# Kernel tuning notes

Hardware: AMD Instinct MI355X
Metric: run time of the kernel (lower is better)

Reference implementation:

```python
import jax, jax.numpy as jnp
import numpy as np

NUM_NODES, NODE_F = 50000, 128
NUM_EDGES, EDGE_F = 500000, 128
B, N = 4096, 100
D = 64      # node_dim
T = 8       # time_dim
LN_EPS = 1e-5


def setup_inputs() -> dict:
    key = jax.random.key(0)
    ks = jax.random.split(key, 16)
    inp = {
        'src_neighbor_node_ids': jax.random.randint(ks[0], (B, N), 0, NUM_NODES),
        'src_neighbor_edge_ids': jax.random.randint(ks[1], (B, N), 0, NUM_EDGES),
        'src_neighbor_times': jax.random.uniform(ks[2], (B, N), dtype=jnp.float32),
        'dst_node_ids': jax.random.randint(ks[3], (B,), 0, NUM_NODES),
        'node_raw_features': jax.random.normal(ks[4], (NUM_NODES, NODE_F), jnp.float32),
        'edge_raw_features': jax.random.normal(ks[5], (NUM_EDGES, EDGE_F), jnp.float32),
        # projection layers (stored as [in, out])
        'W_feat': jax.random.normal(ks[6], (NODE_F, D), jnp.float32) / np.sqrt(NODE_F),
        'b_feat': jnp.zeros((D,), jnp.float32),
        'W_edge': jax.random.normal(ks[7], (1, D), jnp.float32),
        'b_edge': jnp.zeros((D,), jnp.float32),
        'W_time': jax.random.normal(ks[8], (T, D), jnp.float32) / np.sqrt(T),
        'b_time': jnp.zeros((D,), jnp.float32),
        'W_struct': jax.random.normal(ks[9], (1, D), jnp.float32),
        'b_struct': jnp.zeros((D,), jnp.float32),
        # time encoder (cosine basis with log-spaced frequencies)
        'w_tenc': (1.0 / 10 ** np.linspace(0, 9, T)).astype(np.float32),
        'b_tenc': jnp.zeros((T,), jnp.float32),
        # layernorm
        'ln_g': jnp.ones((D,), jnp.float32),
        'ln_b': jnp.zeros((D,), jnp.float32),
        # GCNConv
        'W_gcn': jax.random.normal(ks[10], (D, D), jnp.float32) / np.sqrt(D),
        'b_gcn': jnp.zeros((D,), jnp.float32),
        # output layer
        'W_out': jax.random.normal(ks[11], (D, D), jnp.float32) / np.sqrt(D),
        'b_out': jnp.zeros((D,), jnp.float32),
    }
    return inp


def reference(src_neighbor_node_ids, src_neighbor_edge_ids, src_neighbor_times,
              dst_node_ids, node_raw_features, edge_raw_features,
              W_feat, b_feat, W_edge, b_edge, W_time, b_time, W_struct, b_struct,
              w_tenc, b_tenc, ln_g, ln_b, W_gcn, b_gcn, W_out, b_out):
    f32 = jnp.float32
    nbr_raw = node_raw_features[src_neighbor_node_ids]            # [B,N,F]
    node_f = nbr_raw @ W_feat + b_feat                            # [B,N,D]
    edge_col = edge_raw_features[src_neighbor_edge_ids, 0][..., None]  # [B,N,1]
    edge_f = edge_col @ W_edge + b_edge
    t_enc = jnp.cos(src_neighbor_times[..., None] * w_tenc + b_tenc)   # [B,N,T]
    time_f = t_enc @ W_time + b_time
    co = (src_neighbor_node_ids == dst_node_ids[:, None]).astype(f32)[..., None]
    co_f = co @ W_struct + b_struct
    skill_nbr = nbr_raw[..., 0].astype(jnp.int32)                 # [B,N]
    skill_dst = node_raw_features[dst_node_ids, 0].astype(jnp.int32)  # [B]
    sim = (skill_nbr == skill_dst[:, None]).astype(f32)[..., None]
    sim_f = sim @ W_struct + b_struct
    fused = node_f + edge_f + time_f + co_f + sim_f               # [B,N,D]
    mu = fused.mean(-1, keepdims=True)
    var = ((fused - mu) ** 2).mean(-1, keepdims=True)
    fused = (fused - mu) * jax.lax.rsqrt(var + LN_EPS) * ln_g + ln_b
    # per-sample chain GCN: directed edges j -> j+1 for j in [0, v-2], v = #valid ids,
    # PyG gcn_norm with self loops: deg[j] = 1 + in_degree[j]
    h = fused @ W_gcn                                             # [B,N,D]
    v = (src_neighbor_node_ids > 0).sum(-1)                       # [B]
    pos = jnp.arange(N)[None, :]                                  # [1,N]
    has_in = ((pos >= 1) & (pos < v[:, None])).astype(f32)        # [B,N]
    deg = 1.0 + has_in
    dinv_sqrt = jax.lax.rsqrt(deg)
    h_prev = jnp.pad(h[:, :-1], ((0, 0), (1, 0), (0, 0)))
    d_prev = jnp.pad(dinv_sqrt[:, :-1], ((0, 0), (1, 0)))
    out = h / deg[..., None] + (has_in * d_prev * dinv_sqrt)[..., None] * h_prev + b_gcn
    gnn = jax.nn.relu(out)
    src_emb = gnn.mean(axis=1)                                    # [B,D] global_mean_pool over N
    dst_emb = node_raw_features[dst_node_ids] @ W_feat + b_feat
    src_emb = src_emb @ W_out + b_out
    dst_emb = dst_emb @ W_out + b_out
    return src_emb, dst_emb
```

## Files before the change

### kernel.cpp

```cpp
#include <hip/hip_runtime.h>
#include <stdint.h>

#define NUM_NODES 50000
#define B_ 4096
#define N_ 100

typedef float f32x4 __attribute__((ext_vector_type(4)));
typedef float f32x2 __attribute__((ext_vector_type(2)));
typedef int   i32x4 __attribute__((ext_vector_type(4)));
typedef short s16x8 __attribute__((ext_vector_type(8)));

__device__ inline unsigned short f2bf(float f) {
    unsigned u = __float_as_uint(f);
    u += 0x7fffu + ((u >> 16) & 1u);
    return (unsigned short)(u >> 16);
}

template <int CTRL>
__device__ inline float dpp_add(float x) {
    int t = __builtin_amdgcn_update_dpp(0, __float_as_int(x), CTRL, 0xf, 0xf, true);
    return x + __int_as_float(t);
}
__device__ inline float wave_sum64(float x) {
    x = dpp_add<0x111>(x);
    x = dpp_add<0x112>(x);
    x = dpp_add<0x114>(x);
    x = dpp_add<0x118>(x);
    x = dpp_add<0x142>(x);
    x = dpp_add<0x143>(x);
    return __int_as_float(__builtin_amdgcn_readlane(__float_as_int(x), 63));
}

__global__ __launch_bounds__(256) void k_pre(
    const float* __restrict__ node_raw, const float* __restrict__ W_feat,
    const float* __restrict__ b_feat, const float* __restrict__ W_gcn,
    const float* __restrict__ ln_g, const float* __restrict__ ln_b,
    const float* __restrict__ W_edge, const float* __restrict__ b_edge,
    const float* __restrict__ W_time, const float* __restrict__ b_time,
    const float* __restrict__ W_struct, const float* __restrict__ b_struct,
    float* __restrict__ proj, int* __restrict__ skill,
    float* __restrict__ hb, float* __restrict__ wmg, float* __restrict__ Mg,
    unsigned short* __restrict__ PGmF)
{
    __shared__ float red[4][64];
    __shared__ float PGms[12][64];
    __shared__ unsigned short WfB[16][64][8];
    int blk = blockIdx.x;
    int t = threadIdx.x;
    int dj = t & 63;

    if (blk == gridDim.x - 1) {
        int g = t >> 6;
        float acc = 0.f;
        #pragma unroll
        for (int i = 0; i < 16; ++i) {
            int dk = g * 16 + i;
            acc += ln_b[dk] * W_gcn[dk * 64 + dj];
        }
        red[g][dj] = acc;

        if (t < 64) {
            int d = t;
            float col[11];
            col[0] = W_edge[d];
            col[1] = W_struct[d];
            #pragma unroll
            for (int i = 0; i < 8; ++i) col[2 + i] = W_time[i * 64 + d];
            col[10] = b_edge[d] + b_time[d] + 2.f * b_struct[d];
            float wmv[11];
            #pragma unroll
            for (int j = 0; j < 11; ++j) wmv[j] = wave_sum64(col[j]) * (1.f / 64.f);
            float cc[11];
            #pragma unroll
            for (int j = 0; j < 11; ++j) cc[j] = col[j] - wmv[j];
            #pragma unroll
            for (int j = 0; j < 11; ++j) {
                #pragma unroll
                for (int k = j; k < 11; ++k) {
                    float m = wave_sum64(cc[j] * cc[k]);
                    if (t == 0) { Mg[j * 11 + k] = m; Mg[k * 11 + j] = m; }
                }
            }
            if (t == 0) {
                #pragma unroll
                for (int j = 0; j < 11; ++j) wmg[j] = wmv[j];
            }

            int j = t;
            float accp[12];
            #pragma unroll
            for (int m = 0; m < 12; ++m) accp[m] = 0.f;
            for (int d2 = 0; d2 < 64; ++d2) {
                float gg = ln_g[d2] * W_gcn[d2 * 64 + j];
                float bias_d = b_edge[d2] + b_time[d2] + 2.f * b_struct[d2];
                accp[0] = fmaf(W_edge[d2], gg, accp[0]);
                accp[1] = fmaf(W_struct[d2], gg, accp[1]);
                #pragma unroll
                for (int i = 0; i < 8; ++i)
                    accp[2 + i] = fmaf(W_time[i * 64 + d2], gg, accp[2 + i]);
                accp[10] = fmaf(bias_d, gg, accp[10]);
                accp[11] += gg;
            }
            #pragma unroll
            for (int m = 0; m < 12; ++m) PGms[m][j] = accp[m];
        }
        __syncthreads();
        if (g == 0) hb[dj] = red[0][dj] + red[1][dj] + red[2][dj] + red[3][dj];

        {
            int ct = t >> 6, l = t & 63;
            int col = ct * 16 + (l & 15);
            int ks = (l >> 4) * 8;
            s16x8 a2;
            #pragma unroll
            for (int j2 = 0; j2 < 8; ++j2) {
                int k = ks + j2;
                a2[j2] = (k < 12) ? (short)f2bf(PGms[k][col]) : (short)0;
            }
            *(s16x8*)(PGmF + ((size_t)ct * 64 + l) * 8) = a2;
        }
        return;
    }

    #pragma unroll
    for (int i = 0; i < 4; ++i) {
        int e = t + i * 256;
        int tile = e >> 6;
        int l = e & 63;
        int ct = tile >> 2, kt = tile & 3;
        int col = ct * 16 + (l & 15);
        int ks = kt * 32 + (l >> 4) * 8;
        s16x8 a;
        #pragma unroll
        for (int j = 0; j < 8; ++j)
            a[j] = (short)f2bf(W_feat[(ks + j) * 64 + col]);
        *(s16x8*)&WfB[tile][l][0] = a;
    }
    __syncthreads();

    int w = t >> 6, lane = t & 63;
    int rbase = blk * 64 + w * 16;
    int rA = rbase + (lane & 15);
    int rc = rA < NUM_NODES ? rA : (NUM_NODES - 1);
    int kq = lane >> 4;

    s16x8 A[4];
    float a0x = 0.f;
    #pragma unroll
    for (int kt = 0; kt < 4; ++kt) {
        const float* src = node_raw + (size_t)rc * 128 + kt * 32 + kq * 8;
        f32x4 v0 = *(const f32x4*)src;
        f32x4 v1 = *(const f32x4*)(src + 4);
        s16x8 a;
        a[0] = (short)f2bf(v0.x); a[1] = (short)f2bf(v0.y);
        a[2] = (short)f2bf(v0.z); a[3] = (short)f2bf(v0.w);
        a[4] = (short)f2bf(v1.x); a[5] = (short)f2bf(v1.y);
        a[6] = (short)f2bf(v1.z); a[7] = (short)f2bf(v1.w);
        A[kt] = a;
        if (kt == 0) a0x = v0.x;
    }
    if (kq == 0 && rA < NUM_NODES) skill[rA] = (int)a0x;

    f32x4 acc[4];
    #pragma unroll
    for (int ct = 0; ct < 4; ++ct) { f32x4 z = {0.f,0.f,0.f,0.f}; acc[ct] = z; }
    #pragma unroll
    for (int ct = 0; ct < 4; ++ct) {
        #pragma unroll
        for (int kt = 0; kt < 4; ++kt) {
            s16x8 bfr = *(const s16x8*)&WfB[ct * 4 + kt][lane][0];
            acc[ct] = __builtin_amdgcn_mfma_f32_16x16x32_bf16(A[kt], bfr, acc[ct], 0, 0, 0);
        }
    }
    #pragma unroll
    for (int ct = 0; ct < 4; ++ct) {
        int col = ct * 16 + (lane & 15);
        float bf = b_feat[col];
        #pragma unroll
        for (int j = 0; j < 4; ++j) {
            int row = rbase + kq * 4 + j;
            if (row < NUM_NODES)
                proj[(size_t)row * 64 + col] = acc[ct][j] + bf;
        }
    }
}

__global__ __launch_bounds__(256) void k_pg(
    const float* __restrict__ proj, const float* __restrict__ W_gcn,
    const float* __restrict__ ln_g,
    const float* __restrict__ W_out, const float* __restrict__ b_out,
    const float* __restrict__ W_edge, const float* __restrict__ b_edge,
    const float* __restrict__ W_time, const float* __restrict__ b_time,
    const float* __restrict__ W_struct, const float* __restrict__ b_struct,
    float* __restrict__ projG, float* __restrict__ dstE,
    float* __restrict__ stats)
{
    __shared__ unsigned short WgB[8][64][8];
    __shared__ unsigned short WoB[8][64][8];
    __shared__ unsigned short WsB[2][64][8];
    int t = threadIdx.x;

    #pragma unroll
    for (int i = 0; i < 2; ++i) {
        int e = t + i * 256;
        int tile = e >> 6, l = e & 63;
        int ct = tile >> 1, kt = tile & 1;
        int col = ct * 16 + (l & 15);
        int ks = kt * 32 + (l >> 4) * 8;
        s16x8 a, b2;
        #pragma unroll
        for (int j = 0; j < 8; ++j) {
            int k = ks + j;
            a[j]  = (short)f2bf(ln_g[k] * W_gcn[k * 64 + col]);
            b2[j] = (short)f2bf(W_out[k * 64 + col]);
        }
        *(s16x8*)&WgB[tile][l][0] = a;
        *(s16x8*)&WoB[tile][l][0] = b2;
    }
    if (t < 128) {
        int kt = t >> 6, l = t & 63;
        int col = l & 15;
        int ks = kt * 32 + (l >> 4) * 8;
        s16x8 a;
        #pragma unroll
        for (int j = 0; j < 8; ++j) {
            int d = ks + j;
            float v;
            if (col == 0) v = W_edge[d];
            else if (col == 1) v = W_struct[d];
            else if (col < 10) v = W_time[(col - 2) * 64 + d];
            else if (col == 10) v = b_edge[d] + b_time[d] + 2.f * b_struct[d];
            else if (col == 11) v = 1.f;
            else v = 0.f;
            a[j] = (short)f2bf(v);
        }
        *(s16x8*)&WsB[kt][l][0] = a;
    }
    __syncthreads();

    int w = t >> 6, lane = t & 63;
    int rbase = blockIdx.x * 64 + w * 16;
    int rA = rbase + (lane & 15);
    int rc = rA < NUM_NODES ? rA : (NUM_NODES - 1);
    int kq = lane >> 4;

    s16x8 Ahi[2], Alo[2], Qhi[2], Qlo[2];
    #pragma unroll
    for (int kt = 0; kt < 2; ++kt) {
        const float* src = proj + (size_t)rc * 64 + kt * 32 + kq * 8;
        f32x4 v0 = *(const f32x4*)src;
        f32x4 v1 = *(const f32x4*)(src + 4);
        #pragma unroll
        for (int j = 0; j < 8; ++j) {
            float v = (j < 4) ? v0[j] : v1[j - 4];
            unsigned short hi = f2bf(v);
            float rem = v - __uint_as_float((unsigned)hi << 16);
            Ahi[kt][j] = (short)hi;
            Alo[kt][j] = (short)f2bf(rem);
            float p2 = v * v;
            unsigned short h2 = f2bf(p2);
            float r2 = p2 - __uint_as_float((unsigned)h2 << 16);
            Qhi[kt][j] = (short)h2;
            Qlo[kt][j] = (short)f2bf(r2);
        }
    }

    f32x4 accG[4], accE[4];
    f32x4 accS = {0.f, 0.f, 0.f, 0.f}, accQ = {0.f, 0.f, 0.f, 0.f};
    #pragma unroll
    for (int ct = 0; ct < 4; ++ct) {
        f32x4 z = {0.f, 0.f, 0.f, 0.f};
        accG[ct] = z; accE[ct] = z;
    }
    #pragma unroll
    for (int ct = 0; ct < 4; ++ct) {
        #pragma unroll
        for (int kt = 0; kt < 2; ++kt) {
            s16x8 bg = *(const s16x8*)&WgB[ct * 2 + kt][lane][0];
            accG[ct] = __builtin_amdgcn_mfma_f32_16x16x32_bf16(Alo[kt], bg, accG[ct], 0, 0, 0);
            accG[ct] = __builtin_amdgcn_mfma_f32_16x16x32_bf16(Ahi[kt], bg, accG[ct], 0, 0, 0);
            s16x8 bo = *(const s16x8*)&WoB[ct * 2 + kt][lane][0];
            accE[ct] = __builtin_amdgcn_mfma_f32_16x16x32_bf16(Alo[kt], bo, accE[ct], 0, 0, 0);
            accE[ct] = __builtin_amdgcn_mfma_f32_16x16x32_bf16(Ahi[kt], bo, accE[ct], 0, 0, 0);
        }
    }
    #pragma unroll
    for (int kt = 0; kt < 2; ++kt) {
        s16x8 bs = *(const s16x8*)&WsB[kt][lane][0];
        accS = __builtin_amdgcn_mfma_f32_16x16x32_bf16(Alo[kt], bs, accS, 0, 0, 0);
        accS = __builtin_amdgcn_mfma_f32_16x16x32_bf16(Ahi[kt], bs, accS, 0, 0, 0);
        accQ = __builtin_amdgcn_mfma_f32_16x16x32_bf16(Qlo[kt], bs, accQ, 0, 0, 0);
        accQ = __builtin_amdgcn_mfma_f32_16x16x32_bf16(Qhi[kt], bs, accQ, 0, 0, 0);
    }

    #pragma unroll
    for (int ct = 0; ct < 4; ++ct) {
        int col = ct * 16 + (lane & 15);
        float bo_ = b_out[col];
        #pragma unroll
        for (int j = 0; j < 4; ++j) {
            int row = rbase + kq * 4 + j;
            if (row < NUM_NODES) {
                projG[(size_t)row * 64 + col] = accG[ct][j];
                dstE[(size_t)row * 64 + col] = accE[ct][j] + bo_;
            }
        }
    }
    int c = lane & 15;
    if (c <= 11) {
        #pragma unroll
        for (int j = 0; j < 4; ++j) {
            int row = rbase + kq * 4 + j;
            if (row < NUM_NODES) stats[(size_t)row * 16 + c] = accS[j];
        }
    }
    if (c == 11) {
        #pragma unroll
        for (int j = 0; j < 4; ++j) {
            int row = rbase + kq * 4 + j;
            if (row < NUM_NODES) stats[(size_t)row * 16 + 12] = accQ[j];
        }
    }
}

__global__ __launch_bounds__(512, 8) void k_main(
    const int* __restrict__ ids, const int* __restrict__ eids,
    const float* __restrict__ times, const int* __restrict__ dst_ids,
    const float* __restrict__ edge_raw,
    const float* __restrict__ w_tenc, const float* __restrict__ b_tenc,
    const float* __restrict__ b_gcn, const float* __restrict__ W_out,
    const float* __restrict__ b_out,
    const float* __restrict__ projG, const float* __restrict__ dstE,
    const int* __restrict__ skill,
    const float* __restrict__ hb, const float* __restrict__ wmg,
    const float* __restrict__ Mg, const unsigned short* __restrict__ PGmF,
    const float* __restrict__ stats,
    float* __restrict__ out)
{
    __shared__ unsigned short VA[112 * 32];
    __shared__ float rstd_s[112];
    __shared__ float pooled[2][64];

    int b = blockIdx.x;
    int t = threadIdx.x;
    int lane = t & 63, w = t >> 6;
    int cs = w & 3, rh = w >> 2;

    int dstb = dst_ids[b];

    int idA = ids[b * N_ + lane];
    int idB = ids[b * N_ + (lane < 36 ? 64 + lane : 0)];
    unsigned long long balA = __ballot(idA > 0);
    unsigned long long balB = __ballot((lane < 36) && (idB > 0));
    int v = __popcll(balA) + __popcll(balB);

    int colw = cs * 16 + (lane & 15);
    int kq = lane >> 4;
    float pgv[4][4];
    #pragma unroll
    for (int mt = 0; mt < 4; ++mt) {
        int gt = mt + rh * 3;
        #pragma unroll
        for (int j = 0; j < 4; ++j) {
            int n = gt * 16 + kq * 4 + j;
            int nc = n < N_ ? n : N_ - 1;
            int idn = ids[b * N_ + nc];
            pgv[mt][j] = projG[(size_t)idn * 64 + colw];
        }
    }
    if (w == 7)
        out[(size_t)(B_ + b) * 64 + lane] = dstE[(size_t)dstb * 64 + lane];

    if (t < N_) {
        int skdst = skill[dstb];
        int id_t = ids[b * N_ + t];
        float tm_t = times[b * N_ + t];
        int ei_t = eids[b * N_ + t];
        float e_t = edge_raw[(size_t)ei_t * 128];
        int sk_t = skill[id_t];
        const f32x4* sp4 = (const f32x4*)(stats + (size_t)id_t * 16);
        f32x4 s0 = sp4[0], s1 = sp4[1], s2 = sp4[2];
        float spp = stats[(size_t)id_t * 16 + 12];

        float u[11];
        u[0] = e_t;
        u[1] = (id_t == dstb ? 1.f : 0.f) + (sk_t == skdst ? 1.f : 0.f);
        #pragma unroll
        for (int i = 0; i < 8; ++i) u[2 + i] = __cosf(fmaf(tm_t, w_tenc[i], b_tenc[i]));
        u[10] = 1.f;

        float pwv[11] = {s0.x, s0.y, s0.z, s0.w, s1.x, s1.y, s1.z, s1.w,
                         s2.x, s2.y, s2.z};
        float sp = s2.w;
        float dot_upw = 0.f, su_wm = 0.f;
        #pragma unroll
        for (int j = 0; j < 11; ++j) {
            dot_upw = fmaf(u[j], pwv[j], dot_upw);
            su_wm = fmaf(u[j], wmg[j], su_wm);
        }
        float mu = sp * (1.f / 64.f) + su_wm;
        float q = spp + sp * sp * (1.f / 64.f) + 2.f * dot_upw - 2.f * sp * mu;
        #pragma unroll
        for (int j = 0; j < 11; ++j) {
            float tj = 0.f;
            #pragma unroll
            for (int k = 0; k < 11; ++k) tj = fmaf(Mg[j * 11 + k], u[k], tj);
            q = fmaf(u[j], tj, q);
        }
        float rstd = rsqrtf(fmaxf(q, 0.f) * (1.f / 64.f) + 1e-5f);
        rstd_s[t] = rstd;

        unsigned short vv[32];
        #pragma unroll
        for (int j = 0; j < 11; ++j) vv[j] = f2bf(rstd * u[j]);
        vv[11] = f2bf(-rstd * mu);
        #pragma unroll
        for (int j = 12; j < 32; ++j) vv[j] = 0;
        #pragma unroll
        for (int c = 0; c < 4; ++c)
            *(s16x8*)((char*)VA + t * 64 + ((c ^ (t & 3)) * 16)) = *(const s16x8*)&vv[c * 8];
    } else if (t < 112) {
        rstd_s[t] = 0.f;
        s16x8 z = {0, 0, 0, 0, 0, 0, 0, 0};
        #pragma unroll
        for (int c = 0; c < 4; ++c)
            *(s16x8*)((char*)VA + t * 64 + c * 16) = z;
    }
    __syncthreads();

    s16x8 bfr = *(const s16x8*)(PGmF + ((size_t)cs * 64 + lane) * 8);
    f32x4 acc[4];
    #pragma unroll
    for (int mt = 0; mt < 4; ++mt) {
        int row = (mt + rh * 3) * 16 + (lane & 15);
        s16x8 a = *(const s16x8*)((char*)VA + row * 64 + ((kq ^ (row & 3)) * 16));
        f32x4 z = {0.f, 0.f, 0.f, 0.f};
        acc[mt] = __builtin_amdgcn_mfma_f32_16x16x32_bf16(a, bfr, z, 0, 0, 0);
    }

    float hbv = hb[colw], bgc = b_gcn[colw];
    int plo = rh ? 64 : 0;
    int phi = rh ? N_ : 64;
    float carry = 0.f, po = 0.f;
    #pragma unroll
    for (int mt = 0; mt < 4; ++mt) {
        int nb = (mt + rh * 3) * 16 + kq * 4;
        f32x4 rs4 = *(const f32x4*)&rstd_s[nb];
        float hh[4];
        #pragma unroll
        for (int j = 0; j < 4; ++j)
            hh[j] = fmaf(rs4[j], pgv[mt][j], acc[mt][j]) + hbv;

        float hup = __shfl_up(hh[3], 16, 64);
        float hpj = (kq > 0) ? hup : carry;
        #pragma unroll
        for (int j = 0; j < 4; ++j) {
            int n = nb + j;
            bool hin = (n >= 1) && (n < v);
            float a_ = hin ? 0.5f : 1.f;
            float dprev = (n >= 2 && n <= v) ? 0.70710678118f : 1.f;
            float coef = hin ? dprev * 0.70710678118f : 0.f;
            float o = fmaf(hh[j], a_, fmaf(coef, hpj, bgc));
            po += (n >= plo && n < phi) ? fmaxf(o, 0.f) : 0.f;
            hpj = hh[j];
        }
        carry = __shfl(hh[3], 48 + (lane & 15), 64);
    }
    po += __shfl_xor(po, 16, 64);
    po += __shfl_xor(po, 32, 64);
    if (lane < 16) pooled[rh][colw] = po * (1.f / (float)N_);
    __syncthreads();

    if (w == 0) {
        float o = b_out[lane];
        #pragma unroll
        for (int dk4 = 0; dk4 < 16; ++dk4) {
            f32x4 p0 = *(const f32x4*)&pooled[0][dk4 * 4];
            f32x4 p1 = *(const f32x4*)&pooled[1][dk4 * 4];
            o = fmaf(p0.x + p1.x, W_out[(dk4 * 4 + 0) * 64 + lane], o);
            o = fmaf(p0.y + p1.y, W_out[(dk4 * 4 + 1) * 64 + lane], o);
            o = fmaf(p0.z + p1.z, W_out[(dk4 * 4 + 2) * 64 + lane], o);
            o = fmaf(p0.w + p1.w, W_out[(dk4 * 4 + 3) * 64 + lane], o);
        }
        out[(size_t)b * 64 + lane] = o;
    }
}

extern "C" void kernel_launch(void* const* d_in, const int* in_sizes, int n_in,
                              void* d_out, int out_size, void* d_ws, size_t ws_size,
                              hipStream_t stream)
{
    const int*   ids      = (const int*)d_in[0];
    const int*   eids     = (const int*)d_in[1];
    const float* times    = (const float*)d_in[2];
    const int*   dst_ids  = (const int*)d_in[3];
    const float* node_raw = (const float*)d_in[4];
    const float* edge_raw = (const float*)d_in[5];
    const float* W_feat   = (const float*)d_in[6];
    const float* b_feat   = (const float*)d_in[7];
    const float* W_edge   = (const float*)d_in[8];
    const float* b_edge   = (const float*)d_in[9];
    const float* W_time   = (const float*)d_in[10];
    const float* b_time   = (const float*)d_in[11];
    const float* W_struct = (const float*)d_in[12];
    const float* b_struct = (const float*)d_in[13];
    const float* w_tenc   = (const float*)d_in[14];
    const float* b_tenc   = (const float*)d_in[15];
    const float* ln_g     = (const float*)d_in[16];
    const float* ln_b     = (const float*)d_in[17];
    const float* W_gcn    = (const float*)d_in[18];
    const float* b_gcn    = (const float*)d_in[19];
    const float* W_out    = (const float*)d_in[20];
    const float* b_out    = (const float*)d_in[21];

    char* ws = (char*)d_ws;
    float*          proj   = (float*)ws;
    int*            skill  = (int*)(ws + 12800000);
    float*          hb     = (float*)(ws + 13008192);
    float*          wmg    = (float*)(ws + 13008448);
    float*          Mg     = (float*)(ws + 13008512);
    unsigned short* PGmF   = (unsigned short*)(ws + 13009024);
    float*          stats  = (float*)(ws + 13100032);
    float*          projG  = (float*)(ws + 16400000);
    float*          dstE   = (float*)(ws + 29200000);

    k_pre<<<783, 256, 0, stream>>>(node_raw, W_feat, b_feat, W_gcn, ln_g, ln_b,
                                   W_edge, b_edge, W_time, b_time, W_struct, b_struct,
                                   proj, skill, hb, wmg, Mg, PGmF);
    k_pg<<<782, 256, 0, stream>>>(proj, W_gcn, ln_g, W_out, b_out,
                                  W_edge, b_edge, W_time, b_time, W_struct, b_struct,
                                  projG, dstE, stats);
    k_main<<<B_, 512, 0, stream>>>(ids, eids, times, dst_ids, edge_raw,
                                   w_tenc, b_tenc, b_gcn, W_out, b_out,
                                   projG, dstE, skill, hb, wmg, Mg, PGmF, stats,
                                   (float*)d_out);
}
```

Measured before the change: 81.62 us.

## Map one wave per batch sample in k_main, removing block-wide barriers

Restructures the main kernel so that each 64-lane wave handles a whole sample: 4 samples per 256-thread block, 1024 blocks. Previously 8 waves cooperated on one sample through shared memory and __syncthreads. Each wave now computes per-neighbor stats for its 100 rows, loops over 7 MFMA row tiles for all 4 column tiles, and runs the output projection itself, so no barriers are needed. The projG gathers now happen inside the loop using ids staged in LDS rather than being prefetched up front. This exposes more gather latency per wave and gives less parallelism per sample.

```diff
diff --git a/kernel.cpp b/kernel.cpp
--- a/kernel.cpp
+++ b/kernel.cpp
@@ -323,7 +323,7 @@
     }
 }
 
-__global__ __launch_bounds__(512, 8) void k_main(
+__global__ __launch_bounds__(256, 5) void k_main(
     const int* __restrict__ ids, const int* __restrict__ eids,
     const float* __restrict__ times, const int* __restrict__ dst_ids,
     const float* __restrict__ edge_raw,
@@ -337,153 +337,172 @@
     const float* __restrict__ stats,
     float* __restrict__ out)
 {
-    __shared__ unsigned short VA[112 * 32];
-    __shared__ float rstd_s[112];
-    __shared__ float pooled[2][64];
-
-    int b = blockIdx.x;
+    __shared__ unsigned short VA[4][112][16];
+    __shared__ float rstd_s[4][112];
+    __shared__ int   ids_s[4][112];
+    __shared__ float pooled[4][64];
+
     int t = threadIdx.x;
     int lane = t & 63, w = t >> 6;
-    int cs = w & 3, rh = w >> 2;
+    int b = blockIdx.x * 4 + w;
 
     int dstb = dst_ids[b];
-
-    int idA = ids[b * N_ + lane];
-    int idB = ids[b * N_ + (lane < 36 ? 64 + lane : 0)];
-    unsigned long long balA = __ballot(idA > 0);
-    unsigned long long balB = __ballot((lane < 36) && (idB > 0));
-    int v = __popcll(balA) + __popcll(balB);
-
-    int colw = cs * 16 + (lane & 15);
-    int kq = lane >> 4;
-    float pgv[4][4];
-    #pragma unroll
-    for (int mt = 0; mt < 4; ++mt) {
-        int gt = mt + rh * 3;
+    int skdst = skill[dstb];
+
+    out[(size_t)(B_ + b) * 64 + lane] = dstE[(size_t)dstb * 64 + lane];
+
+    int id0 = ids[b * N_ + lane];
+    bool val1 = lane < (N_ - 64);
+    int id1 = val1 ? ids[b * N_ + 64 + lane] : 0;
+    int v = __popcll(__ballot(id0 > 0)) + __popcll(__ballot(val1 && (id1 > 0)));
+
+    int idr0 = id0, idr1 = id1;
+    #pragma unroll
+    for (int r = 0; r < 2; ++r) {
+        int n = r * 64 + lane;
+        if (n >= 112) continue;
+        if (n < N_) {
+            int id_t = r == 0 ? idr0 : idr1;
+            float tm_t = times[b * N_ + n];
+            int ei_t = eids[b * N_ + n];
+            float e_t = edge_raw[(size_t)ei_t * 128];
+            int sk_t = skill[id_t];
+            const f32x4* sp4 = (const f32x4*)(stats + (size_t)id_t * 16);
+            f32x4 s0 = sp4[0], s1 = sp4[1], s2 = sp4[2];
+            float spp = stats[(size_t)id_t * 16 + 12];
+
+            float u[11];
+            u[0] = e_t;
+            u[1] = (id_t == dstb ? 1.f : 0.f) + (sk_t == skdst ? 1.f : 0.f);
+            #pragma unroll
+            for (int i = 0; i < 8; ++i)
+                u[2 + i] = __cosf(fmaf(tm_t, w_tenc[i], b_tenc[i]));
+            u[10] = 1.f;
+
+            float pwv[11] = {s0.x, s0.y, s0.z, s0.w, s1.x, s1.y, s1.z, s1.w,
+                             s2.x, s2.y, s2.z};
+            float sp = s2.w;
+            float dot_upw = 0.f, su_wm = 0.f;
+            #pragma unroll
+            for (int j = 0; j < 11; ++j) {
+                dot_upw = fmaf(u[j], pwv[j], dot_upw);
+                su_wm = fmaf(u[j], wmg[j], su_wm);
+            }
+            float mu = sp * (1.f / 64.f) + su_wm;
+            float q = spp + sp * sp * (1.f / 64.f) + 2.f * dot_upw - 2.f * sp * mu;
+            #pragma unroll
+            for (int j = 0; j < 11; ++j) {
+                float tj = 0.f;
+                #pragma unroll
+                for (int k = 0; k < 11; ++k) tj = fmaf(Mg[j * 11 + k], u[k], tj);
+                q = fmaf(u[j], tj, q);
+            }
+            float rstd = rsqrtf(fmaxf(q, 0.f) * (1.f / 64.f) + 1e-5f);
+
+            ids_s[w][n] = id_t;
+            rstd_s[w][n] = rstd;
+            unsigned short vv[16];
+            #pragma unroll
+            for (int j = 0; j < 11; ++j) vv[j] = f2bf(rstd * u[j]);
+            vv[11] = f2bf(-rstd * mu);
+            vv[12] = 0; vv[13] = 0; vv[14] = 0; vv[15] = 0;
+            *(s16x8*)&VA[w][n][0] = *(const s16x8*)&vv[0];
+            *(s16x8*)&VA[w][n][8] = *(const s16x8*)&vv[8];
+        } else {
+            ids_s[w][n] = 0;
+            rstd_s[w][n] = 0.f;
+            s16x8 z = {0, 0, 0, 0, 0, 0, 0, 0};
+            *(s16x8*)&VA[w][n][0] = z;
+            *(s16x8*)&VA[w][n][8] = z;
+        }
+    }
+
+    int l15 = lane & 15, kq = lane >> 4;
+    s16x8 bfr0 = *(const s16x8*)(PGmF + ((size_t)0 * 64 + lane) * 8);
+    s16x8 bfr1 = *(const s16x8*)(PGmF + ((size_t)1 * 64 + lane) * 8);
+    s16x8 bfr2 = *(const s16x8*)(PGmF + ((size_t)2 * 64 + lane) * 8);
+    s16x8 bfr3 = *(const s16x8*)(PGmF + ((size_t)3 * 64 + lane) * 8);
+    float hb0 = hb[0 * 16 + l15], hb1 = hb[1 * 16 + l15];
+    float hb2 = hb[2 * 16 + l15], hb3 = hb[3 * 16 + l15];
+    float bg0 = b_gcn[0 * 16 + l15], bg1 = b_gcn[1 * 16 + l15];
+    float bg2 = b_gcn[2 * 16 + l15], bg3 = b_gcn[3 * 16 + l15];
+
+    float po[4] = {0.f, 0.f, 0.f, 0.f};
+    float carry[4] = {0.f, 0.f, 0.f, 0.f};
+
+    for (int mt = 0; mt < 7; ++mt) {
+        int nb = mt * 16 + kq * 4;
+        i32x4 s4 = *(const i32x4*)&ids_s[w][nb];
+        float pgv[4][4];
         #pragma unroll
         for (int j = 0; j < 4; ++j) {
-            int n = gt * 16 + kq * 4 + j;
-            int nc = n < N_ ? n : N_ - 1;
-            int idn = ids[b * N_ + nc];
-            pgv[mt][j] = projG[(size_t)idn * 64 + colw];
-        }
-    }
-    if (w == 7)
-        out[(size_t)(B_ + b) * 64 + lane] = dstE[(size_t)dstb * 64 + lane];
-
-    if (t < N_) {
-        int skdst = skill[dstb];
-        int id_t = ids[b * N_ + t];
-        float tm_t = times[b * N_ + t];
-        int ei_t = eids[b * N_ + t];
-        float e_t = edge_raw[(size_t)ei_t * 128];
-        int sk_t = skill[id_t];
-        const f32x4* sp4 = (const f32x4*)(stats + (size_t)id_t * 16);
-        f32x4 s0 = sp4[0], s1 = sp4[1], s2 = sp4[2];
-        float spp = stats[(size_t)id_t * 16 + 12];
-
-        float u[11];
-        u[0] = e_t;
-        u[1] = (id_t == dstb ? 1.f : 0.f) + (sk_t == skdst ? 1.f : 0.f);
-        #pragma unroll
-        for (int i = 0; i < 8; ++i) u[2 + i] = __cosf(fmaf(tm_t, w_tenc[i], b_tenc[i]));
-        u[10] = 1.f;
-
-        float pwv[11] = {s0.x, s0.y, s0.z, s0.w, s1.x, s1.y, s1.z, s1.w,
-                         s2.x, s2.y, s2.z};
-        float sp = s2.w;
-        float dot_upw = 0.f, su_wm = 0.f;
-        #pragma unroll
-        for (int j = 0; j < 11; ++j) {
-            dot_upw = fmaf(u[j], pwv[j], dot_upw);
-            su_wm = fmaf(u[j], wmg[j], su_wm);
-        }
-        float mu = sp * (1.f / 64.f) + su_wm;
-        float q = spp + sp * sp * (1.f / 64.f) + 2.f * dot_upw - 2.f * sp * mu;
-        #pragma unroll
-        for (int j = 0; j < 11; ++j) {
-            float tj = 0.f;
-            #pragma unroll
-            for (int k = 0; k < 11; ++k) tj = fmaf(Mg[j * 11 + k], u[k], tj);
-            q = fmaf(u[j], tj, q);
-        }
-        float rstd = rsqrtf(fmaxf(q, 0.f) * (1.f / 64.f) + 1e-5f);
-        rstd_s[t] = rstd;
-
-        unsigned short vv[32];
-        #pragma unroll
-        for (int j = 0; j < 11; ++j) vv[j] = f2bf(rstd * u[j]);
-        vv[11] = f2bf(-rstd * mu);
-        #pragma unroll
-        for (int j = 12; j < 32; ++j) vv[j] = 0;
-        #pragma unroll
-        for (int c = 0; c < 4; ++c)
-            *(s16x8*)((char*)VA + t * 64 + ((c ^ (t & 3)) * 16)) = *(const s16x8*)&vv[c * 8];
-    } else if (t < 112) {
-        rstd_s[t] = 0.f;
-        s16x8 z = {0, 0, 0, 0, 0, 0, 0, 0};
-        #pragma unroll
-        for (int c = 0; c < 4; ++c)
-            *(s16x8*)((char*)VA + t * 64 + c * 16) = z;
-    }
-    __syncthreads();
-
-    s16x8 bfr = *(const s16x8*)(PGmF + ((size_t)cs * 64 + lane) * 8);
-    f32x4 acc[4];
-    #pragma unroll
-    for (int mt = 0; mt < 4; ++mt) {
-        int row = (mt + rh * 3) * 16 + (lane & 15);
-        s16x8 a = *(const s16x8*)((char*)VA + row * 64 + ((kq ^ (row & 3)) * 16));
-        f32x4 z = {0.f, 0.f, 0.f, 0.f};
-        acc[mt] = __builtin_amdgcn_mfma_f32_16x16x32_bf16(a, bfr, z, 0, 0, 0);
-    }
-
-    float hbv = hb[colw], bgc = b_gcn[colw];
-    int plo = rh ? 64 : 0;
-    int phi = rh ? N_ : 64;
-    float carry = 0.f, po = 0.f;
-    #pragma unroll
-    for (int mt = 0; mt < 4; ++mt) {
-        int nb = (mt + rh * 3) * 16 + kq * 4;
-        f32x4 rs4 = *(const f32x4*)&rstd_s[nb];
-        float hh[4];
-        #pragma unroll
-        for (int j = 0; j < 4; ++j)
-            hh[j] = fmaf(rs4[j], pgv[mt][j], acc[mt][j]) + hbv;
-
-        float hup = __shfl_up(hh[3], 16, 64);
-        float hpj = (kq > 0) ? hup : carry;
-        #pragma unroll
-        for (int j = 0; j < 4; ++j) {
-            int n = nb + j;
-            bool hin = (n >= 1) && (n < v);
-            float a_ = hin ? 0.5f : 1.f;
-            float dprev = (n >= 2 && n <= v) ? 0.70710678118f : 1.f;
-            float coef = hin ? dprev * 0.70710678118f : 0.f;
-            float o = fmaf(hh[j], a_, fmaf(coef, hpj, bgc));
-            po += (n >= plo && n < phi) ? fmaxf(o, 0.f) : 0.f;
-            hpj = hh[j];
-        }
-        carry = __shfl(hh[3], 48 + (lane & 15), 64);
-    }
-    po += __shfl_xor(po, 16, 64);
-    po += __shfl_xor(po, 32, 64);
-    if (lane < 16) pooled[rh][colw] = po * (1.f / (float)N_);
-    __syncthreads();
-
-    if (w == 0) {
-        float o = b_out[lane];
-        #pragma unroll
-        for (int dk4 = 0; dk4 < 16; ++dk4) {
-            f32x4 p0 = *(const f32x4*)&pooled[0][dk4 * 4];
-            f32x4 p1 = *(const f32x4*)&pooled[1][dk4 * 4];
-            o = fmaf(p0.x + p1.x, W_out[(dk4 * 4 + 0) * 64 + lane], o);
-            o = fmaf(p0.y + p1.y, W_out[(dk4 * 4 + 1) * 64 + lane], o);
-            o = fmaf(p0.z + p1.z, W_out[(dk4 * 4 + 2) * 64 + lane], o);
-            o = fmaf(p0.w + p1.w, W_out[(dk4 * 4 + 3) * 64 + lane], o);
-        }
-        out[(size_t)b * 64 + lane] = o;
-    }
+            const float* pr = projG + (size_t)s4[j] * 64 + l15;
+            pgv[0][j] = pr[0];
+            pgv[1][j] = pr[16];
+            pgv[2][j] = pr[32];
+            pgv[3][j] = pr[48];
+        }
+        f32x4 rs4 = *(const f32x4*)&rstd_s[w][nb];
+
+        int row = mt * 16 + l15;
+        s16x8 a;
+        if (kq < 2) a = *(const s16x8*)&VA[w][row][kq * 8];
+        else { s16x8 z = {0,0,0,0,0,0,0,0}; a = z; }
+        f32x4 zz = {0.f, 0.f, 0.f, 0.f};
+        f32x4 acc0 = __builtin_amdgcn_mfma_f32_16x16x32_bf16(a, bfr0, zz, 0, 0, 0);
+        f32x4 acc1 = __builtin_amdgcn_mfma_f32_16x16x32_bf16(a, bfr1, zz, 0, 0, 0);
+        f32x4 acc2 = __builtin_amdgcn_mfma_f32_16x16x32_bf16(a, bfr2, zz, 0, 0, 0);
+        f32x4 acc3 = __builtin_amdgcn_mfma_f32_16x16x32_bf16(a, bfr3, zz, 0, 0, 0);
+
+        #pragma unroll
+        for (int ct = 0; ct < 4; ++ct) {
+            f32x4 accc = ct == 0 ? acc0 : ct == 1 ? acc1 : ct == 2 ? acc2 : acc3;
+            float hbc = ct == 0 ? hb0 : ct == 1 ? hb1 : ct == 2 ? hb2 : hb3;
+            float bgc = ct == 0 ? bg0 : ct == 1 ? bg1 : ct == 2 ? bg2 : bg3;
+            float hh[4];
+            #pragma unroll
+            for (int j = 0; j < 4; ++j)
+                hh[j] = fmaf(rs4[j], pgv[ct][j], accc[j]) + hbc;
+
+            float hup = __shfl_up(hh[3], 16, 64);
+            float hpj = (kq > 0) ? hup : carry[ct];
+            #pragma unroll
+            for (int j = 0; j < 4; ++j) {
+                int n = nb + j;
+                bool hin = (n >= 1) && (n < v);
+                float a_ = hin ? 0.5f : 1.f;
+                float dprev = (n >= 2 && n <= v) ? 0.70710678118f : 1.f;
+                float coef = hin ? dprev * 0.70710678118f : 0.f;
+                float o = fmaf(hh[j], a_, fmaf(coef, hpj, bgc));
+                po[ct] += (n < N_) ? fmaxf(o, 0.f) : 0.f;
+                hpj = hh[j];
+            }
+            carry[ct] = __shfl(hh[3], 48 + l15, 64);
+        }
+    }
+
+    #pragma unroll
+    for (int ct = 0; ct < 4; ++ct) {
+        po[ct] += __shfl_xor(po[ct], 16, 64);
+        po[ct] += __shfl_xor(po[ct], 32, 64);
+    }
+    if (lane < 16) {
+        pooled[w][0 * 16 + lane] = po[0] * (1.f / (float)N_);
+        pooled[w][1 * 16 + lane] = po[1] * (1.f / (float)N_);
+        pooled[w][2 * 16 + lane] = po[2] * (1.f / (float)N_);
+        pooled[w][3 * 16 + lane] = po[3] * (1.f / (float)N_);
+    }
+
+    float o = b_out[lane];
+    #pragma unroll
+    for (int dk4 = 0; dk4 < 16; ++dk4) {
+        f32x4 p4 = *(const f32x4*)&pooled[w][dk4 * 4];
+        o = fmaf(p4.x, W_out[(dk4 * 4 + 0) * 64 + lane], o);
+        o = fmaf(p4.y, W_out[(dk4 * 4 + 1) * 64 + lane], o);
+        o = fmaf(p4.z, W_out[(dk4 * 4 + 2) * 64 + lane], o);
+        o = fmaf(p4.w, W_out[(dk4 * 4 + 3) * 64 + lane], o);
+    }
+    out[(size_t)b * 64 + lane] = o;
 }
 
 extern "C" void kernel_launch(void* const* d_in, const int* in_sizes, int n_in,
@@ -530,8 +549,8 @@
     k_pg<<<782, 256, 0, stream>>>(proj, W_gcn, ln_g, W_out, b_out,
                                   W_edge, b_edge, W_time, b_time, W_struct, b_struct,
                                   projG, dstE, stats);
-    k_main<<<B_, 512, 0, stream>>>(ids, eids, times, dst_ids, edge_raw,
-                                   w_tenc, b_tenc, b_gcn, W_out, b_out,
-                                   projG, dstE, skill, hb, wmg, Mg, PGmF, stats,
-                                   (float*)d_out);
-}
+    k_main<<<1024, 256, 0, stream>>>(ids, eids, times, dst_ids, edge_raw,
+                                     w_tenc, b_tenc, b_gcn, W_out, b_out,
+                                     projG, dstE, skill, hb, wmg, Mg, PGmF, stats,
+                                     (float*)d_out);
+}
```

Result: slower. 219.1 us (+168.4%).
